# Performance work log

Measured on AMD Instinct MI355X. Metric: run time of the kernel, lower is better.

The kernel has to match this reference:

```python
import jax, jax.numpy as jnp
import numpy as np

K = 3
PAD = 1
EPS = 1e-5


def _conv2d(x, w, b):
    y = jax.lax.conv_general_dilated(x, w, window_strides=(1, 1), padding='SAME',
                                     dimension_numbers=('NCHW', 'OIHW', 'NCHW'))
    return y + b[None, :, None, None]


def _bn(x, g, beta, m, v):
    inv = jax.lax.rsqrt(v + EPS)
    return (x - m[None, :, None, None]) * (g * inv)[None, :, None, None] + beta[None, :, None, None]


def _deform_conv2d(x, offset, w, b):
    # torchvision deform_conv2d (v1, no mask), stride=1, pad=1, 3x3 kernel.
    B, Cin, H, W = x.shape
    Cout = w.shape[0]
    # offset: [B, 2*K*K, H, W] -> (dy, dx) per kernel tap
    off = offset.reshape(B, K * K, 2, H, W)
    dy, dx = off[:, :, 0], off[:, :, 1]                     # [B, K2, H, W]
    ii, jj = jnp.meshgrid(jnp.arange(K), jnp.arange(K), indexing='ij')
    ki = (ii.reshape(-1) - PAD).astype(x.dtype)             # [K2]
    kj = (jj.reshape(-1) - PAD).astype(x.dtype)
    py = jnp.arange(H, dtype=x.dtype)[None, None, :, None] + ki[None, :, None, None] + dy
    px = jnp.arange(W, dtype=x.dtype)[None, None, None, :] + kj[None, :, None, None] + dx
    y0 = jnp.floor(py)
    x0 = jnp.floor(px)
    wy = py - y0
    wx = px - x0
    flat = x.reshape(B, Cin, H * W)

    def gather(yc, xc):
        valid = ((yc >= 0) & (yc < H) & (xc >= 0) & (xc < W)).astype(x.dtype)
        yi = jnp.clip(yc, 0, H - 1).astype(jnp.int32)
        xi = jnp.clip(xc, 0, W - 1).astype(jnp.int32)
        idx = (yi * W + xi).reshape(B, -1)                  # [B, K2*H*W]
        g = jax.vmap(lambda f, i: f[:, i])(flat, idx)       # [B, Cin, K2*H*W]
        return g.reshape(B, Cin, K * K, H, W) * valid[:, None]

    v = (gather(y0,     x0    ) * ((1 - wy) * (1 - wx))[:, None]
         + gather(y0,     x0 + 1) * ((1 - wy) * wx)[:, None]
         + gather(y0 + 1, x0    ) * (wy * (1 - wx))[:, None]
         + gather(y0 + 1, x0 + 1) * (wy * wx)[:, None])     # [B, Cin, K2, H, W]
    out = jnp.einsum('bckhw,ock->bohw', v, w.reshape(Cout, Cin, K * K))
    return out + b[None, :, None, None]


def setup_inputs() -> dict:
    key = jax.random.key(0)
    ks = jax.random.split(key, 12)
    d = {}
    d['x'] = jax.random.normal(ks[0], (32, 3, 64, 64), jnp.float32)
    d['offset1_w'] = jax.random.normal(ks[1], (18, 3, 3, 3), jnp.float32) * 0.05
    d['offset1_b'] = jnp.zeros((18,), jnp.float32)
    d['conv1_w'] = jax.random.normal(ks[2], (64, 3, 3, 3), jnp.float32) * 0.1
    d['conv1_b'] = jnp.zeros((64,), jnp.float32)
    d['bn1_gamma'] = jnp.ones((64,), jnp.float32)
    d['bn1_beta'] = jnp.zeros((64,), jnp.float32)
    d['bn1_mean'] = jnp.zeros((64,), jnp.float32)
    d['bn1_var'] = jax.random.uniform(ks[3], (64,), jnp.float32, 0.5, 1.5)
    d['offset2_w'] = jax.random.normal(ks[4], (18, 64, 3, 3), jnp.float32) * 0.02
    d['offset2_b'] = jnp.zeros((18,), jnp.float32)
    d['conv2_w'] = jax.random.normal(ks[5], (128, 64, 3, 3), jnp.float32) * 0.05
    d['conv2_b'] = jnp.zeros((128,), jnp.float32)
    d['bn2_gamma'] = jnp.ones((128,), jnp.float32)
    d['bn2_beta'] = jnp.zeros((128,), jnp.float32)
    d['bn2_mean'] = jnp.zeros((128,), jnp.float32)
    d['bn2_var'] = jax.random.uniform(ks[6], (128,), jnp.float32, 0.5, 1.5)
    d['fc1_w'] = jax.random.normal(ks[7], (256, 128), jnp.float32) * 0.08
    d['fc1_b'] = jnp.zeros((256,), jnp.float32)
    d['fc2_w'] = jax.random.normal(ks[8], (200, 256), jnp.float32) * 0.06
    d['fc2_b'] = jnp.zeros((200,), jnp.float32)
    return d


def reference(x, offset1_w, offset1_b, conv1_w, conv1_b, bn1_gamma, bn1_beta, bn1_mean, bn1_var,
              offset2_w, offset2_b, conv2_w, conv2_b, bn2_gamma, bn2_beta, bn2_mean, bn2_var,
              fc1_w, fc1_b, fc2_w, fc2_b):
    # Eval-mode forward (dropout layers are identity / deterministic).
    off1 = _conv2d(x, offset1_w, offset1_b)
    h = _deform_conv2d(x, off1, conv1_w, conv1_b)
    h = jax.nn.relu(_bn(h, bn1_gamma, bn1_beta, bn1_mean, bn1_var))
    off2 = _conv2d(h, offset2_w, offset2_b)
    h = _deform_conv2d(h, off2, conv2_w, conv2_b)
    h = jax.nn.relu(_bn(h, bn2_gamma, bn2_beta, bn2_mean, bn2_var))
    h = h.mean(axis=(2, 3))                                 # global avg pool -> [B, 128]
    h = jax.nn.relu(h @ fc1_w.T + fc1_b)
    return h @ fc2_w.T + fc2_b
```

## Files before the change

kernel.cpp:

```cpp
#include <hip/hip_runtime.h>

#define EPS 1e-5f

#define W1OT 0
#define W1T  1024
#define W2T  4096
#define W2OB 40960
#define SC1  59392
#define SH1  59456
#define SC2  59520
#define SH2  59648
#define POOL 59776
#define XP   65536
#define H1B  589824
#define W2T_U   8192
#define W2OB_U  81920
#define H1B_U   1179648

typedef __attribute__((ext_vector_type(8))) short bhalf8;
typedef __attribute__((ext_vector_type(8))) unsigned short u16x8;
typedef __attribute__((ext_vector_type(4))) float f32x4;

#define BPAD 72
#define OPAD 584

struct Tap { int i00, i01, i10, i11; float w00, w01, w10, w11; };

__device__ __forceinline__ Tap make_tap(float py, float px) {
    float y0f = floorf(py), x0f = floorf(px);
    float wy = py - y0f, wx = px - x0f;
    bool by0 = (y0f >= 0.f)  && (y0f < 64.f);
    bool by1 = (y0f >= -1.f) && (y0f < 63.f);
    bool bx0 = (x0f >= 0.f)  && (x0f < 64.f);
    bool bx1 = (x0f >= -1.f) && (x0f < 63.f);
    int y0 = min(max((int)y0f, 0), 63);
    int y1 = min(max((int)y0f + 1, 0), 63);
    int x0 = min(max((int)x0f, 0), 63);
    int x1 = min(max((int)x0f + 1, 0), 63);
    Tap tp;
    tp.i00 = y0 * 64 + x0; tp.i01 = y0 * 64 + x1;
    tp.i10 = y1 * 64 + x0; tp.i11 = y1 * 64 + x1;
    tp.w00 = (by0 && bx0) ? (1.f - wy) * (1.f - wx) : 0.f;
    tp.w01 = (by0 && bx1) ? (1.f - wy) * wx         : 0.f;
    tp.w10 = (by1 && bx0) ? wy * (1.f - wx)         : 0.f;
    tp.w11 = (by1 && bx1) ? wy * wx                 : 0.f;
    return tp;
}

__device__ __forceinline__ ushort f2bf(float f) {
    union { float f; uint u; } a; a.f = f;
    uint u = a.u;
    return (ushort)((u + 0x7fffu + ((u >> 16) & 1u)) >> 16);
}
__device__ __forceinline__ float bf2f(ushort u) {
    union { uint u; float f; } a; a.u = ((uint)u) << 16;
    return a.f;
}

__global__ __launch_bounds__(256) void k_prep(
    const float* __restrict__ x,
    const float* __restrict__ o1w, const float* __restrict__ c1w,
    const float* __restrict__ o2w, const float* __restrict__ c2w,
    const float* __restrict__ c1b, const float* __restrict__ g1,
    const float* __restrict__ be1, const float* __restrict__ m1,
    const float* __restrict__ v1,
    const float* __restrict__ c2b, const float* __restrict__ g2,
    const float* __restrict__ be2, const float* __restrict__ m2,
    const float* __restrict__ v2,
    float* __restrict__ ws) {
    int tid = blockIdx.x * 256 + threadIdx.x;
    ushort* wsu = (ushort*)ws;
    if (tid < 648) {
        int co = tid % 18, tc = tid / 18, c = tc & 3, t = tc >> 2;
        ws[W1OT + tid] = (c < 3) ? o1w[(co * 3 + c) * 9 + t] : 0.f;
    } else if (tid < 2952) {
        int i = tid - 648;
        int co = i & 63, tc = i >> 6, c = tc & 3, t = tc >> 2;
        ws[W1T + i] = (c < 3) ? c1w[(co * 3 + c) * 9 + t] : 0.f;
    } else if (tid < 76680) {
        int i = tid - 2952;
        int c = i & 63, n = (i >> 6) & 127, t = i >> 13;
        wsu[W2T_U + i] = f2bf(c2w[(n * 64 + c) * 9 + t]);
    } else if (tid < 95112) {
        int i = tid - 76680;
        int n = i / 576, k = i - n * 576;
        int c = k & 63, t = k >> 6;
        float v = (n < 18) ? o2w[(n * 64 + c) * 9 + t] : 0.f;
        wsu[W2OB_U + i] = f2bf(v);
    } else if (tid < 95176) {
        int i = tid - 95112;
        float s = g1[i] * rsqrtf(v1[i] + EPS);
        ws[SC1 + i] = s;
        ws[SH1 + i] = (c1b[i] - m1[i]) * s + be1[i];
    } else if (tid < 95304) {
        int i = tid - 95176;
        float s = g2[i] * rsqrtf(v2[i] + EPS);
        ws[SC2 + i] = s;
        ws[SH2 + i] = (c2b[i] - m2[i]) * s + be2[i];
    } else if (tid < 99400) {
        ws[POOL + tid - 95304] = 0.f;
    } else if (tid < 230472) {
        int i = tid - 99400;
        int b = i >> 12, hw = i & 4095;
        const float* xpp = x + (size_t)b * 3 * 4096 + hw;
        f32x4 o;
        o[0] = xpp[0]; o[1] = xpp[4096]; o[2] = xpp[8192]; o[3] = 0.f;
        *(f32x4*)(ws + XP + (size_t)i * 4) = o;
    }
}

__global__ __launch_bounds__(256, 3) void k_def1(
    const float* __restrict__ o1b, float* __restrict__ ws) {
    __shared__ float wo[648];
    __shared__ float wt[2304];
    for (int i = threadIdx.x; i < 648; i += 256) wo[i] = ws[W1OT + i];
    for (int i = threadIdx.x; i < 2304; i += 256) wt[i] = ws[W1T + i];
    __syncthreads();
    int tid = blockIdx.x * 256 + threadIdx.x;
    int b = tid >> 12, hw = tid & 4095, h = hw >> 6, w = hw & 63;
    const float* xp = ws + XP + (size_t)b * 16384;
    float off[18];
#pragma unroll
    for (int i = 0; i < 18; ++i) off[i] = o1b[i];
#pragma unroll
    for (int t = 0; t < 9; ++t) {
        int yy = h + t / 3 - 1, xx = w + t % 3 - 1;
        f32x4 pv = (f32x4)0.f;
        if (yy >= 0 && yy < 64 && xx >= 0 && xx < 64)
            pv = *(const f32x4*)(xp + (yy * 64 + xx) * 4);
#pragma unroll
        for (int c = 0; c < 3; ++c) {
            const float* wp = wo + (t * 4 + c) * 18;
#pragma unroll
            for (int co = 0; co < 18; ++co) off[co] += pv[c] * wp[co];
        }
    }
    f32x4 v[9];
#pragma unroll
    for (int t = 0; t < 9; ++t) {
        Tap tp = make_tap((float)(h + t / 3 - 1) + off[2 * t],
                          (float)(w + t % 3 - 1) + off[2 * t + 1]);
        f32x4 c00 = *(const f32x4*)(xp + tp.i00 * 4);
        f32x4 c01 = *(const f32x4*)(xp + tp.i01 * 4);
        f32x4 c10 = *(const f32x4*)(xp + tp.i10 * 4);
        f32x4 c11 = *(const f32x4*)(xp + tp.i11 * 4);
        v[t] = tp.w00 * c00 + tp.w01 * c01 + tp.w10 * c10 + tp.w11 * c11;
    }
    const float* sc = ws + SC1;
    const float* sh = ws + SH1;
    ushort* op = (ushort*)ws + H1B_U + (size_t)(b * 4096 + hw) * 64;
#pragma unroll
    for (int ch = 0; ch < 2; ++ch) {
        float acc[32];
#pragma unroll
        for (int i = 0; i < 32; ++i) acc[i] = 0.f;
#pragma unroll
        for (int t = 0; t < 9; ++t)
#pragma unroll
            for (int c = 0; c < 3; ++c) {
                float vk = v[t][c];
                const float* wp = wt + (t * 4 + c) * 64 + ch * 32;
#pragma unroll
                for (int co = 0; co < 32; ++co) acc[co] += vk * wp[co];
            }
        ushort ob[32];
#pragma unroll
        for (int i = 0; i < 32; ++i) {
            int co = ch * 32 + i;
            ob[i] = f2bf(fmaxf(acc[i] * sc[co] + sh[co], 0.f));
        }
#pragma unroll
        for (int i = 0; i < 4; ++i)
            *(uint4*)(op + ch * 32 + i * 8) = *(const uint4*)(ob + i * 8);
    }
}

__global__ __launch_bounds__(256, 4) void k_def2(
    const float* __restrict__ o2b, float* __restrict__ ws) {
    __shared__ ushort smem[32 * OPAD];
    float* offL = (float*)smem;
    ushort* Bdef = smem + 2304;
    int g = blockIdx.x;
    int b = (g & 7) * 4 + ((g >> 3) & 3);
    int row = g >> 5;
    int tid = threadIdx.x, lane = tid & 63, wv = tid >> 6;
    int r = lane & 15, q = lane >> 4;
    int px = wv * 16 + r;
    const ushort* hb = (const ushort*)ws + H1B_U + (size_t)b * 262144;
    const ushort* wB = (const ushort*)ws + W2T_U;
    const ushort* bt = (const ushort*)ws + W2OB_U;

    for (int i = tid; i < 2304; i += 256) {
        int n = i / 72, kk = (i - n * 72) * 8;
        *(uint4*)(smem + n * OPAD + kk) = *(const uint4*)(bt + n * 576 + kk);
    }
    __syncthreads();

    f32x4 acc2[2];
    acc2[0] = (f32x4)0.f; acc2[1] = (f32x4)0.f;
#pragma unroll
    for (int t = 0; t < 9; ++t) {
        int yy = row + t / 3 - 1;
        int xx = px + t % 3 - 1;
        bool val = (yy >= 0 && yy < 64 && xx >= 0 && xx < 64);
        int yyc = min(max(yy, 0), 63), xxc = min(max(xx, 0), 63);
        const ushort* ap = hb + (size_t)(yyc * 64 + xxc) * 64 + q * 8;
#pragma unroll
        for (int ks = 0; ks < 2; ++ks) {
            bhalf8 af = val ? *(const bhalf8*)(ap + ks * 32) : (bhalf8)(short)0;
            int kk = t * 64 + ks * 32 + q * 8;
#pragma unroll
            for (int nt = 0; nt < 2; ++nt) {
                bhalf8 bf = *(const bhalf8*)(smem + (nt * 16 + r) * OPAD + kk);
                acc2[nt] = __builtin_amdgcn_mfma_f32_16x16x32_bf16(af, bf, acc2[nt], 0, 0, 0);
            }
        }
    }
    __syncthreads();
#pragma unroll
    for (int nt = 0; nt < 2; ++nt) {
        int n = nt * 16 + r;
        if (n < 18) {
            float bias = o2b[n];
#pragma unroll
            for (int rr = 0; rr < 4; ++rr)
                offL[(wv * 16 + q * 4 + rr) * 18 + n] = acc2[nt][rr] + bias;
        }
    }
    __syncthreads();

    f32x4 acc[8];
#pragma unroll
    for (int j = 0; j < 8; ++j) acc[j] = (f32x4)0.f;
    int bn = tid >> 1, bc = (tid & 1) * 32;

    for (int t = 0; t < 9; ++t) {
        float oy = offL[px * 18 + 2 * t];
        float ox = offL[px * 18 + 2 * t + 1];
        Tap tp = make_tap((float)(row + t / 3 - 1) + oy,
                          (float)(px + t % 3 - 1) + ox);
        if (t) __syncthreads();
        {
            const uint4* s4 = (const uint4*)(wB + (t * 128 + bn) * 64 + bc);
            uint4 p0 = s4[0], p1 = s4[1], p2 = s4[2], p3 = s4[3];
            ushort* dst = Bdef + bn * BPAD + bc;
            *(uint4*)(dst)      = p0;
            *(uint4*)(dst + 8)  = p1;
            *(uint4*)(dst + 16) = p2;
            *(uint4*)(dst + 24) = p3;
        }
        __syncthreads();
#pragma unroll
        for (int ks = 0; ks < 2; ++ks) {
            int ko = ks * 32 + q * 8;
            bhalf8 bf[8];
#pragma unroll
            for (int nt = 0; nt < 8; ++nt)
                bf[nt] = *(const bhalf8*)(Bdef + (nt * 16 + r) * BPAD + ko);
            u16x8 g00 = *(const u16x8*)(hb + (size_t)tp.i00 * 64 + ko);
            u16x8 g01 = *(const u16x8*)(hb + (size_t)tp.i01 * 64 + ko);
            u16x8 g10 = *(const u16x8*)(hb + (size_t)tp.i10 * 64 + ko);
            u16x8 g11 = *(const u16x8*)(hb + (size_t)tp.i11 * 64 + ko);
            f32x4 lo = (f32x4)0.f, hi = (f32x4)0.f;
#pragma unroll
            for (int j = 0; j < 4; ++j) {
                lo[j] = tp.w00 * bf2f(g00[j]) + tp.w01 * bf2f(g01[j])
                      + tp.w10 * bf2f(g10[j]) + tp.w11 * bf2f(g11[j]);
                hi[j] = tp.w00 * bf2f(g00[j + 4]) + tp.w01 * bf2f(g01[j + 4])
                      + tp.w10 * bf2f(g10[j + 4]) + tp.w11 * bf2f(g11[j + 4]);
            }
            bhalf8 af;
#pragma unroll
            for (int j = 0; j < 4; ++j) {
                af[j]     = (short)f2bf(lo[j]);
                af[j + 4] = (short)f2bf(hi[j]);
            }
#pragma unroll
            for (int nt = 0; nt < 8; ++nt)
                acc[nt] = __builtin_amdgcn_mfma_f32_16x16x32_bf16(af, bf[nt], acc[nt], 0, 0, 0);
        }
    }
    const float* sc = ws + SC2;
    const float* sh = ws + SH2;
    float* pool = ws + POOL;
#pragma unroll
    for (int nt = 0; nt < 8; ++nt) {
        int col = nt * 16 + r;
        float s0 = sc[col], s1 = sh[col];
        float s = 0.f;
#pragma unroll
        for (int rr = 0; rr < 4; ++rr)
            s += fmaxf(acc[nt][rr] * s0 + s1, 0.f);
        s += __shfl_xor(s, 16);
        s += __shfl_xor(s, 32);
        if (lane < 16) atomicAdd(&pool[b * 128 + col], s);
    }
}

__global__ __launch_bounds__(256) void k_fc(
    const float* __restrict__ w1, const float* __restrict__ b1,
    const float* __restrict__ w2, const float* __restrict__ b2,
    const float* __restrict__ ws, float* __restrict__ out) {
    int b = blockIdx.x, o = threadIdx.x;
    __shared__ float pl[128];
    __shared__ float hl[256];
    if (o < 128) pl[o] = ws[POOL + b * 128 + o] * (1.f / 4096.f);
    __syncthreads();
    float s = b1[o];
    const float* wp = w1 + o * 128;
#pragma unroll 8
    for (int c = 0; c < 128; ++c) s += pl[c] * wp[c];
    hl[o] = fmaxf(s, 0.f);
    __syncthreads();
    if (o < 200) {
        float s2 = b2[o];
        const float* wp2 = w2 + o * 256;
#pragma unroll 8
        for (int c = 0; c < 256; ++c) s2 += hl[c] * wp2[c];
        out[b * 200 + o] = s2;
    }
}

extern "C" void kernel_launch(void* const* d_in, const int* in_sizes, int n_in,
                              void* d_out, int out_size, void* d_ws, size_t ws_size,
                              hipStream_t stream) {
    const float* x   = (const float*)d_in[0];
    const float* o1w = (const float*)d_in[1];
    const float* o1b = (const float*)d_in[2];
    const float* c1w = (const float*)d_in[3];
    const float* c1b = (const float*)d_in[4];
    const float* g1  = (const float*)d_in[5];
    const float* be1 = (const float*)d_in[6];
    const float* m1  = (const float*)d_in[7];
    const float* v1  = (const float*)d_in[8];
    const float* o2w = (const float*)d_in[9];
    const float* o2b = (const float*)d_in[10];
    const float* c2w = (const float*)d_in[11];
    const float* c2b = (const float*)d_in[12];
    const float* g2  = (const float*)d_in[13];
    const float* be2 = (const float*)d_in[14];
    const float* m2  = (const float*)d_in[15];
    const float* v2  = (const float*)d_in[16];
    const float* f1w = (const float*)d_in[17];
    const float* f1b = (const float*)d_in[18];
    const float* f2w = (const float*)d_in[19];
    const float* f2b = (const float*)d_in[20];
    float* ws  = (float*)d_ws;
    float* out = (float*)d_out;

    k_prep<<<901, 256, 0, stream>>>(x, o1w, c1w, o2w, c2w,
                                    c1b, g1, be1, m1, v1,
                                    c2b, g2, be2, m2, v2, ws);
    k_def1<<<512, 256, 0, stream>>>(o1b, ws);
    k_def2<<<2048, 256, 0, stream>>>(o2b, ws);
    k_fc<<<32, 256, 0, stream>>>(f1w, f1b, f2w, f2b, ws, out);
}
```

Measured before the change: 301.9 us.

## Run first deformable conv projection on bf16 MFMA instead of scalar FMAs

```diff
diff --git a/kernel.cpp b/kernel.cpp
--- a/kernel.cpp
+++ b/kernel.cpp
@@ -3,7 +3,7 @@
 #define EPS 1e-5f
 
 #define W1OT 0
-#define W1T  1024
+#define W1B  1024
 #define W2T  4096
 #define W2OB 40960
 #define SC1  59392
@@ -13,6 +13,7 @@
 #define POOL 59776
 #define XP   65536
 #define H1B  589824
+#define W1B_U   2048
 #define W2T_U   8192
 #define W2OB_U  81920
 #define H1B_U   1179648
@@ -23,6 +24,7 @@
 
 #define BPAD 72
 #define OPAD 584
+#define APAD 40
 
 struct Tap { int i00, i01, i10, i11; float w00, w01, w10, w11; };
 
@@ -73,34 +75,36 @@
     if (tid < 648) {
         int co = tid % 18, tc = tid / 18, c = tc & 3, t = tc >> 2;
         ws[W1OT + tid] = (c < 3) ? o1w[(co * 3 + c) * 9 + t] : 0.f;
-    } else if (tid < 2952) {
+    } else if (tid < 2696) {
         int i = tid - 648;
-        int co = i & 63, tc = i >> 6, c = tc & 3, t = tc >> 2;
-        ws[W1T + i] = (c < 3) ? c1w[(co * 3 + c) * 9 + t] : 0.f;
-    } else if (tid < 76680) {
-        int i = tid - 2952;
+        int n = i >> 5, k = i & 31;
+        float v = 0.f;
+        if (k < 27) { int c = k % 3, t = k / 3; v = c1w[(n * 3 + c) * 9 + t]; }
+        wsu[W1B_U + i] = f2bf(v);
+    } else if (tid < 76424) {
+        int i = tid - 2696;
         int c = i & 63, n = (i >> 6) & 127, t = i >> 13;
         wsu[W2T_U + i] = f2bf(c2w[(n * 64 + c) * 9 + t]);
-    } else if (tid < 95112) {
-        int i = tid - 76680;
+    } else if (tid < 94856) {
+        int i = tid - 76424;
         int n = i / 576, k = i - n * 576;
         int c = k & 63, t = k >> 6;
         float v = (n < 18) ? o2w[(n * 64 + c) * 9 + t] : 0.f;
         wsu[W2OB_U + i] = f2bf(v);
-    } else if (tid < 95176) {
-        int i = tid - 95112;
+    } else if (tid < 94920) {
+        int i = tid - 94856;
         float s = g1[i] * rsqrtf(v1[i] + EPS);
         ws[SC1 + i] = s;
         ws[SH1 + i] = (c1b[i] - m1[i]) * s + be1[i];
-    } else if (tid < 95304) {
-        int i = tid - 95176;
+    } else if (tid < 95048) {
+        int i = tid - 94920;
         float s = g2[i] * rsqrtf(v2[i] + EPS);
         ws[SC2 + i] = s;
         ws[SH2 + i] = (c2b[i] - m2[i]) * s + be2[i];
-    } else if (tid < 99400) {
-        ws[POOL + tid - 95304] = 0.f;
-    } else if (tid < 230472) {
-        int i = tid - 99400;
+    } else if (tid < 99144) {
+        ws[POOL + tid - 95048] = 0.f;
+    } else if (tid < 230216) {
+        int i = tid - 99144;
         int b = i >> 12, hw = i & 4095;
         const float* xpp = x + (size_t)b * 3 * 4096 + hw;
         f32x4 o;
@@ -109,19 +113,33 @@
     }
 }
 
-__global__ __launch_bounds__(256, 3) void k_def1(
+__global__ __launch_bounds__(256, 4) void k_def1(
     const float* __restrict__ o1b, float* __restrict__ ws) {
+    __shared__ ushort Alds[256 * APAD];
+    __shared__ ushort Blds[64 * APAD];
     __shared__ float wo[648];
-    __shared__ float wt[2304];
-    for (int i = threadIdx.x; i < 648; i += 256) wo[i] = ws[W1OT + i];
-    for (int i = threadIdx.x; i < 2304; i += 256) wt[i] = ws[W1T + i];
-    __syncthreads();
-    int tid = blockIdx.x * 256 + threadIdx.x;
-    int b = tid >> 12, hw = tid & 4095, h = hw >> 6, w = hw & 63;
+    __shared__ float scl[128];
+    int tid = threadIdx.x;
+    for (int i = tid; i < 648; i += 256) wo[i] = ws[W1OT + i];
+    if (tid < 128) scl[tid] = ws[SC1 + tid];
+    {
+        const ushort* src = (const ushort*)ws + W1B_U;
+        if (tid < 128) {
+            int n = tid >> 1, half = (tid & 1) * 16;
+            *(uint4*)(Blds + n * APAD + half)     = *(const uint4*)(src + n * 32 + half);
+            *(uint4*)(Blds + n * APAD + half + 8) = *(const uint4*)(src + n * 32 + half + 8);
+        }
+    }
+    int g = blockIdx.x;
+    int b = (g & 7) * 4 + ((g >> 3) & 3);
+    int row0 = (g >> 5) * 4;
+    int h = row0 + (tid >> 6), w = tid & 63;
     const float* xp = ws + XP + (size_t)b * 16384;
+
     float off[18];
 #pragma unroll
     for (int i = 0; i < 18; ++i) off[i] = o1b[i];
+    __syncthreads();
 #pragma unroll
     for (int t = 0; t < 9; ++t) {
         int yy = h + t / 3 - 1, xx = w + t % 3 - 1;
@@ -135,7 +153,9 @@
             for (int co = 0; co < 18; ++co) off[co] += pv[c] * wp[co];
         }
     }
-    f32x4 v[9];
+    ushort ob[32];
+#pragma unroll
+    for (int i = 0; i < 32; ++i) ob[i] = 0;
 #pragma unroll
     for (int t = 0; t < 9; ++t) {
         Tap tp = make_tap((float)(h + t / 3 - 1) + off[2 * t],
@@ -144,34 +164,46 @@
         f32x4 c01 = *(const f32x4*)(xp + tp.i01 * 4);
         f32x4 c10 = *(const f32x4*)(xp + tp.i10 * 4);
         f32x4 c11 = *(const f32x4*)(xp + tp.i11 * 4);
-        v[t] = tp.w00 * c00 + tp.w01 * c01 + tp.w10 * c10 + tp.w11 * c11;
-    }
-    const float* sc = ws + SC1;
-    const float* sh = ws + SH1;
-    ushort* op = (ushort*)ws + H1B_U + (size_t)(b * 4096 + hw) * 64;
-#pragma unroll
-    for (int ch = 0; ch < 2; ++ch) {
-        float acc[32];
-#pragma unroll
-        for (int i = 0; i < 32; ++i) acc[i] = 0.f;
-#pragma unroll
-        for (int t = 0; t < 9; ++t)
-#pragma unroll
-            for (int c = 0; c < 3; ++c) {
-                float vk = v[t][c];
-                const float* wp = wt + (t * 4 + c) * 64 + ch * 32;
-#pragma unroll
-                for (int co = 0; co < 32; ++co) acc[co] += vk * wp[co];
-            }
-        ushort ob[32];
-#pragma unroll
-        for (int i = 0; i < 32; ++i) {
-            int co = ch * 32 + i;
-            ob[i] = f2bf(fmaxf(acc[i] * sc[co] + sh[co], 0.f));
-        }
+        f32x4 vt = tp.w00 * c00 + tp.w01 * c01 + tp.w10 * c10 + tp.w11 * c11;
+        ob[t * 3 + 0] = f2bf(vt[0]);
+        ob[t * 3 + 1] = f2bf(vt[1]);
+        ob[t * 3 + 2] = f2bf(vt[2]);
+    }
+    {
+        ushort* ar = Alds + tid * APAD;
 #pragma unroll
         for (int i = 0; i < 4; ++i)
-            *(uint4*)(op + ch * 32 + i * 8) = *(const uint4*)(ob + i * 8);
+            *(uint4*)(ar + i * 8) = *(const uint4*)(ob + i * 8);
+    }
+    __syncthreads();
+
+    int lane = tid & 63, wv = tid >> 6;
+    int r = lane & 15, q = lane >> 4;
+    bhalf8 bf[4];
+#pragma unroll
+    for (int nt = 0; nt < 4; ++nt)
+        bf[nt] = *(const bhalf8*)(Blds + (nt * 16 + r) * APAD + q * 8);
+    f32x4 acc[4][4];
+#pragma unroll
+    for (int mt = 0; mt < 4; ++mt) {
+        bhalf8 af = *(const bhalf8*)(Alds + (wv * 64 + mt * 16 + r) * APAD + q * 8);
+#pragma unroll
+        for (int nt = 0; nt < 4; ++nt)
+            acc[mt][nt] = __builtin_amdgcn_mfma_f32_16x16x32_bf16(af, bf[nt], (f32x4)0.f, 0, 0, 0);
+    }
+    ushort* hb = (ushort*)ws + H1B_U + (size_t)(b * 4096 + row0 * 64) * 64;
+#pragma unroll
+    for (int nt = 0; nt < 4; ++nt) {
+        int col = nt * 16 + r;
+        float s0 = scl[col], s1 = scl[64 + col];
+#pragma unroll
+        for (int mt = 0; mt < 4; ++mt) {
+            int pxl = wv * 64 + mt * 16 + q * 4;
+#pragma unroll
+            for (int rr = 0; rr < 4; ++rr)
+                hb[(size_t)(pxl + rr) * 64 + col] =
+                    f2bf(fmaxf(acc[mt][nt][rr] * s0 + s1, 0.f));
+        }
     }
 }
 
@@ -348,7 +380,7 @@
     float* ws  = (float*)d_ws;
     float* out = (float*)d_out;
 
-    k_prep<<<901, 256, 0, stream>>>(x, o1w, c1w, o2w, c2w,
+    k_prep<<<900, 256, 0, stream>>>(x, o1w, c1w, o2w, c2w,
                                     c1b, g1, be1, m1, v1,
                                     c2b, g2, be2, m2, v2, ws);
     k_def1<<<512, 256, 0, stream>>>(o1b, ws);
```

New measurement: 290.2 us. -3.9%, faster.
